# Optimization experiments

Measured on AMD Instinct MI355X. Metric: run time of the kernel, lower is better.

The kernel has to match this reference:

```python
import jax, jax.numpy as jnp
import numpy as np

B, T, H, V, S = 64, 32, 512, 32000, 400


def setup_inputs() -> dict:
    key = jax.random.key(0)
    ks = jax.random.split(key, 14)
    f = lambda k, s: jax.random.normal(k, s, dtype=jnp.float32)
    return {
        "inputs": jax.random.randint(ks[0], (B, T), 0, V),
        "embedding0": f(ks[1], (B, H)),
        "output0": f(ks[2], (B, H)),
        "tree_h0": f(ks[3], (B, H)),
        "tree_c0": f(ks[4], (B, H)),
        "tree_context": f(ks[5], (B, S, H)),
        "text_h0": f(ks[6], (B, H)),
        "text_c0": f(ks[7], (B, H)),
        "text_context": f(ks[8], (B, S, H)),
        "word_emb": f(ks[9], (V, H)) * 0.02,
        "Wx": f(ks[10], (2 * H, 4 * H)) * 0.02,   # LSTM input weights (input_size = 2H)
        "Wh": f(ks[11], (H, 4 * H)) * 0.02,       # LSTM recurrent weights
        "b": jnp.zeros((4 * H,), jnp.float32),
        "W_in": f(ks[12], (H, H)) * 0.02,         # attention score projection
        "W_out": f(ks[13], (4 * H, H)) * 0.02,    # attention combine projection
    }


def _lstm_cell(x, h, c, Wx, Wh, b):
    g = x @ Wx + h @ Wh + b                      # [B,4H]
    i, f, gg, o = jnp.split(g, 4, axis=-1)
    c_new = jax.nn.sigmoid(f) * c + jax.nn.sigmoid(i) * jnp.tanh(gg)
    h_new = jax.nn.sigmoid(o) * jnp.tanh(c_new)
    return h_new, c_new


def _attend(h, ctx, W_in):
    target = h @ W_in                             # [B,H]
    scores = jnp.einsum('bsh,bh->bs', ctx, target)
    attn = jax.nn.softmax(scores, axis=-1)
    return jnp.einsum('bs,bsh->bh', attn, ctx)    # weighted context [B,H]


def reference(inputs, embedding0, output0, tree_h0, tree_c0, tree_context,
              text_h0, text_c0, text_context, word_emb, Wx, Wh, b, W_in, W_out):
    embeddings = word_emb[inputs]                 # [B,T,H]
    embeddings = jnp.transpose(embeddings, (1, 0, 2))  # time-major [T,B,H]

    def step(carry, emb_i):
        emb, out, th, tc, xh, xc = carry
        x = jnp.concatenate([emb, out], axis=1)   # [B,2H]
        th, tc = _lstm_cell(x, th, tc, Wx, Wh, b)  # tree branch (shared weights)
        xh, xc = _lstm_cell(x, xh, xc, Wx, Wh, b)  # text branch (shared weights)
        w_tree = _attend(th, tree_context, W_in)
        w_text = _attend(xh, text_context, W_in)
        combined = jnp.concatenate([w_tree, w_text, th, xh], axis=1)  # [B,4H]
        out = jnp.tanh(combined @ W_out)           # dropout = identity (eval mode)
        return (emb_i, out, th, tc, xh, xc), out

    carry0 = (embedding0, output0, tree_h0, tree_c0, text_h0, text_c0)
    _, outs = jax.lax.scan(step, carry0, embeddings)  # outs: [T,B,H]
    return jnp.transpose(outs, (1, 0, 2))             # [B,T,H]
```

## Files before the change

kernel.cpp:

```cpp
#include <hip/hip_runtime.h>
#include <hip/hip_bf16.h>
#include <math.h>

#define BB 64
#define TT 32
#define HH 512
#define H2 1024
#define H4 2048
#define SS 400

#define OFF_WT_HI 0u
#define OFF_WT_LO 1572864u
#define OFF_WIT_HI 3145728u
#define OFF_WIT_LO 3276800u
#define OFF_EH    3407872u
#define OFF_EL    3932160u
#define OFF_OH    4456448u
#define OFF_OL    4472832u
#define OFF_HHP   4489216u
#define OFF_HLP   4521984u
#define OFF_TC    4554752u
#define OFF_XC    4620288u
#define OFF_TH    4685824u
#define OFF_XH    4751360u
#define OFF_G     4816896u
#define OFF_TGTP  6914048u
#define OFF_PACC  7438336u
#define OFF_PML   7962624u
#define OFF_CTX16 7964672u
#define WS_NEED_F 21071872u
#define OFF_WOT_HI 21071872u
#define OFF_WOT_LO 21596160u
#define OFF_COMBH  22120448u
#define OFF_COMBL  22153216u
#define WS_NEED2_F 22185984u
#define OFF_PART  OFF_G

typedef short bf16x8 __attribute__((ext_vector_type(8)));
typedef float f32x4  __attribute__((ext_vector_type(4)));

__device__ __forceinline__ float sigm(float x){ return 1.f/(1.f+__expf(-x)); }

__device__ __forceinline__ unsigned short bf_rn(float x){
  unsigned int u = __float_as_uint(x);
  return (unsigned short)((u + 0x7fffu + ((u>>16)&1u)) >> 16);
}
__device__ __forceinline__ void split2(float x, unsigned short &h, unsigned short &l){
  h = bf_rn(x);
  float hf = __uint_as_float(((unsigned int)h)<<16);
  l = bf_rn(x - hf);
}
__device__ __forceinline__ float blo(unsigned int u){ return __uint_as_float(u<<16); }
__device__ __forceinline__ float bhi(unsigned int u){ return __uint_as_float(u & 0xffff0000u); }

__global__ __launch_bounds__(256) void k_wprep(const float* __restrict__ Wx,
    const float* __restrict__ Wh, unsigned short* __restrict__ wt_hi,
    unsigned short* __restrict__ wt_lo){
  __shared__ float lds[64][68];
  int bk = blockIdx.x >> 5, bn = blockIdx.x & 31;
  int k0 = bk*64, n0 = bn*64;
  int tid = threadIdx.x;
  #pragma unroll
  for (int i=0;i<4;i++){
    int flat = tid + i*256;
    int k = flat >> 4, nq = flat & 15;
    int kg = k0 + k;
    const float* srow = (kg < 1024) ? Wx + (size_t)kg*H4 : Wh + (size_t)(kg-1024)*H4;
    float4 v = *(const float4*)(srow + n0 + nq*4);
    *(float4*)&lds[k][nq*4] = v;
  }
  __syncthreads();
  #pragma unroll
  for (int i=0;i<2;i++){
    int flat = tid + i*256;
    int n = flat >> 3, k8 = flat & 7;
    ushort4 h0, h1, l0, l1;
    unsigned short h[8], l[8];
    #pragma unroll
    for (int j=0;j<8;j++) split2(lds[k8*8+j][n], h[j], l[j]);
    h0.x=h[0];h0.y=h[1];h0.z=h[2];h0.w=h[3]; h1.x=h[4];h1.y=h[5];h1.z=h[6];h1.w=h[7];
    l0.x=l[0];l0.y=l[1];l0.z=l[2];l0.w=l[3]; l1.x=l[4];l1.y=l[5];l1.z=l[6];l1.w=l[7];
    size_t dst = (size_t)(n0+n)*1536 + k0 + k8*8;
    *(ushort4*)(wt_hi+dst) = h0; *(ushort4*)(wt_hi+dst+4) = h1;
    *(ushort4*)(wt_lo+dst) = l0; *(ushort4*)(wt_lo+dst+4) = l1;
  }
}

__global__ __launch_bounds__(256) void k_wiprep(const float* __restrict__ W_in,
    unsigned short* __restrict__ wit_hi, unsigned short* __restrict__ wit_lo){
  __shared__ float lds[64][68];
  int bk = blockIdx.x >> 3, bn = blockIdx.x & 7;
  int k0 = bk*64, n0 = bn*64;
  int tid = threadIdx.x;
  #pragma unroll
  for (int i=0;i<4;i++){
    int flat = tid + i*256;
    int k = flat >> 4, nq = flat & 15;
    float4 v = *(const float4*)(W_in + (size_t)(k0+k)*HH + n0 + nq*4);
    *(float4*)&lds[k][nq*4] = v;
  }
  __syncthreads();
  #pragma unroll
  for (int i=0;i<2;i++){
    int flat = tid + i*256;
    int n = flat >> 3, k8 = flat & 7;
    ushort4 h0, h1, l0, l1;
    unsigned short h[8], l[8];
    #pragma unroll
    for (int j=0;j<8;j++) split2(lds[k8*8+j][n], h[j], l[j]);
    h0.x=h[0];h0.y=h[1];h0.z=h[2];h0.w=h[3]; h1.x=h[4];h1.y=h[5];h1.z=h[6];h1.w=h[7];
    l0.x=l[0];l0.y=l[1];l0.z=l[2];l0.w=l[3]; l1.x=l[4];l1.y=l[5];l1.z=l[6];l1.w=l[7];
    size_t dst = (size_t)(n0+n)*HH + k0 + k8*8;
    *(ushort4*)(wit_hi+dst) = h0; *(ushort4*)(wit_hi+dst+4) = h1;
    *(ushort4*)(wit_lo+dst) = l0; *(ushort4*)(wit_lo+dst+4) = l1;
  }
}

__global__ __launch_bounds__(256) void k_woprep(const float* __restrict__ W_out,
    unsigned short* __restrict__ wot_hi, unsigned short* __restrict__ wot_lo){
  __shared__ float lds[64][68];
  int bk = blockIdx.x >> 3, bn = blockIdx.x & 7;
  int k0 = bk*64, n0 = bn*64;
  int tid = threadIdx.x;
  #pragma unroll
  for (int i=0;i<4;i++){
    int flat = tid + i*256;
    int k = flat >> 4, nq = flat & 15;
    float4 v = *(const float4*)(W_out + (size_t)(k0+k)*HH + n0 + nq*4);
    *(float4*)&lds[k][nq*4] = v;
  }
  __syncthreads();
  #pragma unroll
  for (int i=0;i<2;i++){
    int flat = tid + i*256;
    int n = flat >> 3, k8 = flat & 7;
    ushort4 h0, h1, l0, l1;
    unsigned short h[8], l[8];
    #pragma unroll
    for (int j=0;j<8;j++) split2(lds[k8*8+j][n], h[j], l[j]);
    h0.x=h[0];h0.y=h[1];h0.z=h[2];h0.w=h[3]; h1.x=h[4];h1.y=h[5];h1.z=h[6];h1.w=h[7];
    l0.x=l[0];l0.y=l[1];l0.z=l[2];l0.w=l[3]; l1.x=l[4];l1.y=l[5];l1.z=l[6];l1.w=l[7];
    size_t dst = (size_t)(n0+n)*H4 + k0 + k8*8;
    *(ushort4*)(wot_hi+dst) = h0; *(ushort4*)(wot_hi+dst+4) = h1;
    *(ushort4*)(wot_lo+dst) = l0; *(ushort4*)(wot_lo+dst+4) = l1;
  }
}

__global__ __launch_bounds__(256) void k_ctx16(const float* __restrict__ trctx,
    const float* __restrict__ txctx, unsigned short* __restrict__ ctx16){
  size_t gid = (size_t)blockIdx.x*256 + threadIdx.x;
  size_t off = gid*8;
  const size_t CH = (size_t)BB*SS*HH;
  const float* src = (off < CH) ? trctx + off : txctx + (off - CH);
  float4 a = *(const float4*)src;
  float4 c = *(const float4*)(src+4);
  ushort4 u0, u1;
  u0.x=bf_rn(a.x); u0.y=bf_rn(a.y); u0.z=bf_rn(a.z); u0.w=bf_rn(a.w);
  u1.x=bf_rn(c.x); u1.y=bf_rn(c.y); u1.z=bf_rn(c.z); u1.w=bf_rn(c.w);
  *(ushort4*)(ctx16+off) = u0;
  *(ushort4*)(ctx16+off+4) = u1;
}

__global__ __launch_bounds__(128) void k_prep(const int* __restrict__ inp,
    const float* __restrict__ emb0, const float* __restrict__ wemb,
    unsigned short* __restrict__ eh, unsigned short* __restrict__ el){
  int n = blockIdx.x; int t = n >> 6, b = n & 63;
  const float* src = (t==0) ? emb0 + (size_t)b*HH
                            : wemb + (size_t)inp[b*TT + (t-1)]*HH;
  float4 v = ((const float4*)src)[threadIdx.x];
  ushort4 h, l;
  split2(v.x,h.x,l.x); split2(v.y,h.y,l.y); split2(v.z,h.z,l.z); split2(v.w,h.w,l.w);
  size_t base = ((size_t)t*BB + b)*HH + threadIdx.x*4;
  *(ushort4*)(eh+base) = h; *(ushort4*)(el+base) = l;
}

__global__ __launch_bounds__(256) void k_init(const float* __restrict__ th0,
    const float* __restrict__ tc0, const float* __restrict__ xh0,
    const float* __restrict__ xc0, const float* __restrict__ out0,
    float* __restrict__ ws){
  unsigned short* hhp = (unsigned short*)(ws + OFF_HHP);
  unsigned short* hlp = (unsigned short*)(ws + OFF_HLP);
  unsigned short* oh  = (unsigned short*)(ws + OFF_OH);
  unsigned short* ol  = (unsigned short*)(ws + OFF_OL);
  int which = blockIdx.x >> 5;
  int idx = (blockIdx.x & 31)*256 + threadIdx.x;
  if (which==0){ ((float4*)(ws+OFF_TC))[idx] = ((const float4*)tc0)[idx]; return; }
  if (which==1){ ((float4*)(ws+OFF_XC))[idx] = ((const float4*)xc0)[idx]; return; }
  const float* s = which==2? th0 : which==3? xh0 : out0;
  float4 v = ((const float4*)s)[idx];
  ushort4 h, l;
  split2(v.x,h.x,l.x); split2(v.y,h.y,l.y); split2(v.z,h.z,l.z); split2(v.w,h.w,l.w);
  if (which==4){
    *(ushort4*)(oh + (size_t)idx*4) = h; *(ushort4*)(ol + (size_t)idx*4) = l;
  } else {
    size_t base = (size_t)(which-2)*BB*HH + (size_t)idx*4;
    *(ushort4*)(hhp+base) = h; *(ushort4*)(hlp+base) = l;
  }
}

__global__ __launch_bounds__(256) void k_gemm(const unsigned short* __restrict__ wt_hi,
    const unsigned short* __restrict__ wt_lo, const unsigned short* __restrict__ eh,
    const unsigned short* __restrict__ el, const unsigned short* __restrict__ oh,
    const unsigned short* __restrict__ ol, const unsigned short* __restrict__ hhp,
    const unsigned short* __restrict__ hlp, float* __restrict__ gpart, int t){
  int tid = threadIdx.x, lane = tid & 63, wave = tid >> 6;
  int bn = blockIdx.x & 31, ks = blockIdx.x >> 5;
  int lm = lane & 15, lk = (lane >> 4) << 3;
  f32x4 acc[2][4];
  #pragma unroll
  for (int i=0;i<2;i++)
    #pragma unroll
    for (int j=0;j<4;j++) acc[i][j] = (f32x4){0.f,0.f,0.f,0.f};
  size_t ebase[2], obase[2], hbase[2];
  #pragma unroll
  for (int i=0;i<2;i++){
    int r = (wave*2 + i)*16 + lm;
    int b = r & 63, br = r >> 6;
    ebase[i] = ((size_t)t*BB + b)*HH;
    obase[i] = (size_t)b*HH;
    hbase[i] = ((size_t)br*BB + b)*HH;
  }
  size_t wb[4];
  #pragma unroll
  for (int j=0;j<4;j++) wb[j] = (size_t)(bn*64 + j*16 + lm)*1536;
  #pragma unroll
  for (int c=0;c<6;c++){
    int kc = ks*192 + c*32;
    int sec = kc >> 9;
    int kk = (kc & 511) + lk;
    const unsigned short* ph = sec==0? eh : sec==1? oh : hhp;
    const unsigned short* pl = sec==0? el : sec==1? ol : hlp;
    bf16x8 ah[2], al[2], wh_[4], wl_[4];
    #pragma unroll
    for (int i=0;i<2;i++){
      size_t off = (sec==0? ebase[i] : sec==1? obase[i] : hbase[i]) + kk;
      ah[i] = *(const bf16x8*)(ph + off);
      al[i] = *(const bf16x8*)(pl + off);
    }
    int kw = kc + lk;
    #pragma unroll
    for (int j=0;j<4;j++){
      wh_[j] = *(const bf16x8*)(wt_hi + wb[j] + kw);
      wl_[j] = *(const bf16x8*)(wt_lo + wb[j] + kw);
    }
    #pragma unroll
    for (int i=0;i<2;i++)
      #pragma unroll
      for (int j=0;j<4;j++){
        acc[i][j] = __builtin_amdgcn_mfma_f32_16x16x32_bf16(ah[i], wh_[j], acc[i][j], 0,0,0);
        acc[i][j] = __builtin_amdgcn_mfma_f32_16x16x32_bf16(ah[i], wl_[j], acc[i][j], 0,0,0);
        acc[i][j] = __builtin_amdgcn_mfma_f32_16x16x32_bf16(al[i], wh_[j], acc[i][j], 0,0,0);
      }
  }
  int lr4 = (lane >> 4) * 4;
  #pragma unroll
  for (int i=0;i<2;i++){
    int m0 = (wave*2+i)*16;
    #pragma unroll
    for (int j=0;j<4;j++){
      int col = bn*64 + j*16 + lm;
      #pragma unroll
      for (int q=0;q<4;q++){
        int row = m0 + lr4 + q;
        gpart[((size_t)ks*128 + row)*H4 + col] = acc[i][j][q];
      }
    }
  }
}

__global__ __launch_bounds__(256) void k_lstm(float* __restrict__ ws,
    const float* __restrict__ bias, int rs){
  int gid = blockIdx.x*256 + threadIdx.x;
  int b = gid >> 9, j = gid & 511;
  int wsl = rs ^ 1;
  const float* gp = ws + OFF_G;
  unsigned short* hhp = (unsigned short*)(ws + OFF_HHP);
  unsigned short* hlp = (unsigned short*)(ws + OFF_HLP);
  #pragma unroll
  for (int br=0;br<2;br++){
    float g0=0.f,g1=0.f,g2=0.f,g3=0.f;
    #pragma unroll
    for (int ks=0;ks<8;ks++){
      size_t base = ((size_t)ks*128 + br*64 + b)*H4 + j;
      g0 += gp[base]; g1 += gp[base+512]; g2 += gp[base+1024]; g3 += gp[base+1536];
    }
    g0 += bias[j]; g1 += bias[512+j]; g2 += bias[1024+j]; g3 += bias[1536+j];
    size_t hoff = (br? OFF_XH : OFF_TH), coff = (br? OFF_XC : OFF_TC);
    float cold = ws[coff + (size_t)rs*BB*HH + (size_t)b*HH + j];
    float cn = sigm(g1)*cold + sigm(g0)*tanhf(g2);
    float hn = sigm(g3)*tanhf(cn);
    ws[coff + (size_t)wsl*BB*HH + (size_t)b*HH + j] = cn;
    ws[hoff + (size_t)wsl*BB*HH + (size_t)b*HH + j] = hn;
    unsigned short h_, l_;
    split2(hn, h_, l_);
    hhp[(size_t)(br*64+b)*HH + j] = h_;
    hlp[(size_t)(br*64+b)*HH + j] = l_;
  }
}

__global__ __launch_bounds__(256) void k_tgtB(const unsigned short* __restrict__ wit_hi,
    const unsigned short* __restrict__ wit_lo, const unsigned short* __restrict__ hhp,
    const unsigned short* __restrict__ hlp, float* __restrict__ tgtp){
  int tid = threadIdx.x, lane = tid & 63, wave = tid >> 6;
  int cn = blockIdx.x & 7, ks = blockIdx.x >> 3;
  int lm = lane & 15, lk = (lane >> 4) << 3;
  f32x4 acc[2][4];
  #pragma unroll
  for (int i=0;i<2;i++)
    #pragma unroll
    for (int j=0;j<4;j++) acc[i][j] = (f32x4){0.f,0.f,0.f,0.f};
  size_t abase[2];
  #pragma unroll
  for (int i=0;i<2;i++) abase[i] = (size_t)(wave*32 + i*16 + lm)*HH;
  size_t wb[4];
  #pragma unroll
  for (int j=0;j<4;j++) wb[j] = (size_t)(cn*64 + j*16 + lm)*HH;
  #pragma unroll
  for (int c=0;c<2;c++){
    int kc = ks*64 + c*32;
    bf16x8 ah[2], al[2], wh_[4], wl_[4];
    #pragma unroll
    for (int i=0;i<2;i++){
      ah[i] = *(const bf16x8*)(hhp + abase[i] + kc + lk);
      al[i] = *(const bf16x8*)(hlp + abase[i] + kc + lk);
    }
    #pragma unroll
    for (int j=0;j<4;j++){
      wh_[j] = *(const bf16x8*)(wit_hi + wb[j] + kc + lk);
      wl_[j] = *(const bf16x8*)(wit_lo + wb[j] + kc + lk);
    }
    #pragma unroll
    for (int i=0;i<2;i++)
      #pragma unroll
      for (int j=0;j<4;j++){
        acc[i][j] = __builtin_amdgcn_mfma_f32_16x16x32_bf16(ah[i], wh_[j], acc[i][j], 0,0,0);
        acc[i][j] = __builtin_amdgcn_mfma_f32_16x16x32_bf16(ah[i], wl_[j], acc[i][j], 0,0,0);
        acc[i][j] = __builtin_amdgcn_mfma_f32_16x16x32_bf16(al[i], wh_[j], acc[i][j], 0,0,0);
      }
  }
  int lr4 = (lane >> 4) * 4;
  #pragma unroll
  for (int i=0;i<2;i++){
    int m0 = wave*32 + i*16;
    #pragma unroll
    for (int j=0;j<4;j++){
      int col = cn*64 + j*16 + lm;
      #pragma unroll
      for (int q=0;q<4;q++){
        int row = m0 + lr4 + q;
        tgtp[((size_t)ks*128 + row)*HH + col] = acc[i][j][q];
      }
    }
  }
}

__global__ __launch_bounds__(512, 8) void k_attn(const float* __restrict__ tree_ctx,
    const float* __restrict__ text_ctx, const unsigned short* __restrict__ ctx16,
    float* __restrict__ ws, int use16){
  int blk = blockIdx.x;
  int sh = blk & 7, b = (blk>>3) & 63, branch = blk >> 9;
  int tid = threadIdx.x, lane = tid & 63, wave = tid >> 6;
  __shared__ float tgt_s[512];
  __shared__ float sc_s[64];
  __shared__ float w_s[64];
  __shared__ float accs[8][512];
  int row128 = branch*64 + b;
  if (tid < 128){
    float4 s = {0,0,0,0};
    #pragma unroll
    for (int p=0;p<8;p++){
      float4 v = *(const float4*)(ws + OFF_TGTP + ((size_t)p*128 + row128)*HH + tid*4);
      s.x += v.x; s.y += v.y; s.z += v.z; s.w += v.w;
    }
    ((float4*)tgt_s)[tid] = s;
  }
  if (tid >= 128 && tid < 192) sc_s[tid-128] = -INFINITY;
  __syncthreads();
  const size_t CH = (size_t)BB*SS*HH;
  const float* ctxf = (branch? text_ctx : tree_ctx) + ((size_t)b*SS + sh*50)*HH;
  const unsigned short* c16 = ctx16 + (branch? CH:0) + ((size_t)b*SS + sh*50)*HH;
  float4 ta = *(const float4*)&tgt_s[lane*8];
  float4 tb = *(const float4*)&tgt_s[lane*8+4];
  if (use16){
    for (int r = wave; r < 50; r += 8){
      uint4 u = *(const uint4*)(c16 + (size_t)r*HH + lane*8);
      float p = blo(u.x)*ta.x + bhi(u.x)*ta.y + blo(u.y)*ta.z + bhi(u.y)*ta.w
              + blo(u.z)*tb.x + bhi(u.z)*tb.y + blo(u.w)*tb.z + bhi(u.w)*tb.w;
      #pragma unroll
      for (int off=32; off; off>>=1) p += __shfl_xor(p, off, 64);
      if (lane==0) sc_s[r] = p;
    }
  } else {
    for (int r = wave; r < 50; r += 8){
      const float* crow = ctxf + (size_t)r*HH + lane*8;
      float4 ca = *(const float4*)crow;
      float4 cb = *(const float4*)(crow+4);
      float p = ca.x*ta.x + ca.y*ta.y + ca.z*ta.z + ca.w*ta.w
              + cb.x*tb.x + cb.y*tb.y + cb.z*tb.z + cb.w*tb.w;
      #pragma unroll
      for (int off=32; off; off>>=1) p += __shfl_xor(p, off, 64);
      if (lane==0) sc_s[r] = p;
    }
  }
  __syncthreads();
  if (wave==0){
    float s = sc_s[lane];
    float m = s;
    #pragma unroll
    for (int off=32; off; off>>=1) m = fmaxf(m, __shfl_xor(m, off, 64));
    float e = (lane<50)? __expf(s-m) : 0.f;
    w_s[lane] = e;
    float l = e;
    #pragma unroll
    for (int off=32; off; off>>=1) l += __shfl_xor(l, off, 64);
    if (lane==0){
      int pidx = (branch*64 + b)*8 + sh;
      ws[OFF_PML + (size_t)pidx*2]   = m;
      ws[OFF_PML + (size_t)pidx*2+1] = l;
    }
  }
  __syncthreads();
  float a[8] = {0,0,0,0,0,0,0,0};
  if (use16){
    for (int r = wave; r < 50; r += 8){
      float w = w_s[r];
      uint4 u = *(const uint4*)(c16 + (size_t)r*HH + lane*8);
      a[0] += w*blo(u.x); a[1] += w*bhi(u.x);
      a[2] += w*blo(u.y); a[3] += w*bhi(u.y);
      a[4] += w*blo(u.z); a[5] += w*bhi(u.z);
      a[6] += w*blo(u.w); a[7] += w*bhi(u.w);
    }
  } else {
    for (int r = wave; r < 50; r += 8){
      float w = w_s[r];
      const float* crow = ctxf + (size_t)r*HH + lane*8;
      float4 ca = *(const float4*)crow;
      float4 cb = *(const float4*)(crow+4);
      a[0] += w*ca.x; a[1] += w*ca.y; a[2] += w*ca.z; a[3] += w*ca.w;
      a[4] += w*cb.x; a[5] += w*cb.y; a[6] += w*cb.z; a[7] += w*cb.w;
    }
  }
  #pragma unroll
  for (int j=0;j<8;j++) accs[wave][lane*8+j] = a[j];
  __syncthreads();
  float s = 0.f;
  #pragma unroll
  for (int w8=0;w8<8;w8++) s += accs[w8][tid];
  int pidx = (branch*64 + b)*8 + sh;
  ws[OFF_PACC + (size_t)pidx*HH + tid] = s;
}

__global__ __launch_bounds__(256) void k_outA(float* __restrict__ ws){
  __shared__ float ce_s[2][8];
  int b = blockIdx.x, tid = threadIdx.x;
  if (tid < 2){
    int p0 = (tid*64 + b)*8;
    float mv[8], lv[8];
    float M = -INFINITY;
    #pragma unroll
    for (int i=0;i<8;i++){
      mv[i] = ws[OFF_PML + (size_t)(p0+i)*2];
      lv[i] = ws[OFF_PML + (size_t)(p0+i)*2+1];
      M = fmaxf(M, mv[i]);
    }
    float L = 0.f, ev[8];
    #pragma unroll
    for (int i=0;i<8;i++){ ev[i] = __expf(mv[i]-M); L += lv[i]*ev[i]; }
    #pragma unroll
    for (int i=0;i<8;i++) ce_s[tid][i] = ev[i]/L;
  }
  __syncthreads();
  int h = tid*4;
  int sec = h >> 9, hs = h & 511;
  int p0 = (sec*64 + b)*8;
  float4 v = {0,0,0,0};
  #pragma unroll
  for (int p=0;p<8;p++){
    float4 a = *(const float4*)(ws + OFF_PACC + (size_t)(p0+p)*HH + hs);
    float cw = ce_s[sec][p];
    v.x += a.x*cw; v.y += a.y*cw; v.z += a.z*cw; v.w += a.w*cw;
  }
  ushort4 hv, lv;
  split2(v.x,hv.x,lv.x); split2(v.y,hv.y,lv.y); split2(v.z,hv.z,lv.z); split2(v.w,hv.w,lv.w);
  unsigned short* ch = (unsigned short*)(ws + OFF_COMBH);
  unsigned short* cl = (unsigned short*)(ws + OFF_COMBL);
  *(ushort4*)(ch + (size_t)b*1024 + h) = hv;
  *(ushort4*)(cl + (size_t)b*1024 + h) = lv;
}

__global__ __launch_bounds__(256) void k_outBm(const unsigned short* __restrict__ wot_hi,
    const unsigned short* __restrict__ wot_lo, const unsigned short* __restrict__ combh,
    const unsigned short* __restrict__ combl, const unsigned short* __restrict__ hhp,
    const unsigned short* __restrict__ hlp, float* __restrict__ part){
  int tid = threadIdx.x, lane = tid & 63, wave = tid >> 6;
  int nt = blockIdx.x & 7, ks = blockIdx.x >> 3;
  int lm = lane & 15, lk = (lane >> 4) << 3;
  f32x4 acc[4];
  #pragma unroll
  for (int m=0;m<4;m++) acc[m] = (f32x4){0.f,0.f,0.f,0.f};
  size_t wb = (size_t)(nt*64 + wave*16 + lm)*H4;
  #pragma unroll
  for (int c=0;c<8;c++){
    int kg = ks*256 + c*32;
    int sec = kg >> 9;
    bf16x8 wh_ = *(const bf16x8*)(wot_hi + wb + kg + lk);
    bf16x8 wl_ = *(const bf16x8*)(wot_lo + wb + kg + lk);
    #pragma unroll
    for (int m=0;m<4;m++){
      int row = m*16 + lm;
      bf16x8 ah, al;
      if (sec < 2){
        size_t off = (size_t)row*1024 + kg + lk;
        ah = *(const bf16x8*)(combh + off);
        al = *(const bf16x8*)(combl + off);
      } else {
        size_t off = ((size_t)(sec-2)*64 + row)*HH + (kg & 511) + lk;
        ah = *(const bf16x8*)(hhp + off);
        al = *(const bf16x8*)(hlp + off);
      }
      acc[m] = __builtin_amdgcn_mfma_f32_16x16x32_bf16(ah, wh_, acc[m], 0,0,0);
      acc[m] = __builtin_amdgcn_mfma_f32_16x16x32_bf16(ah, wl_, acc[m], 0,0,0);
      acc[m] = __builtin_amdgcn_mfma_f32_16x16x32_bf16(al, wh_, acc[m], 0,0,0);
    }
  }
  int lr4 = (lane >> 4) * 4;
  int col = nt*64 + wave*16 + lm;
  #pragma unroll
  for (int m=0;m<4;m++){
    #pragma unroll
    for (int q=0;q<4;q++){
      int b = m*16 + lr4 + q;
      part[((size_t)ks*BB + b)*HH + col] = acc[m][q];
    }
  }
}

__global__ __launch_bounds__(256) void k_outB(const float* __restrict__ W_out,
    float* __restrict__ ws, int wsl){
  __shared__ float comb_s[16][256];
  __shared__ float ce_s[16][8];
  int tid = threadIdx.x, lane = tid & 63, wave = tid >> 6;
  int blk = blockIdx.x;
  int ct = blk & 7, bg = (blk>>3)&3, ks = blk>>5;
  int b0 = bg*16;
  int k0 = ks*256;
  int sec = ks >> 1;
  int kk0 = (ks & 1)*256;
  int c = ct*64 + lane;
  if (sec < 2){
    if (tid < 16){
      int b = b0 + tid;
      int p0 = (sec*64 + b)*8;
      float mv[8], lv[8];
      float M = -INFINITY;
      #pragma unroll
      for (int i=0;i<8;i++){
        mv[i] = ws[OFF_PML + (size_t)(p0+i)*2];
        lv[i] = ws[OFF_PML + (size_t)(p0+i)*2+1];
        M = fmaxf(M, mv[i]);
      }
      float L = 0.f, ev[8];
      #pragma unroll
      for (int i=0;i<8;i++){ ev[i] = __expf(mv[i]-M); L += lv[i]*ev[i]; }
      #pragma unroll
      for (int i=0;i<8;i++) ce_s[tid][i] = ev[i]/L;
    }
    __syncthreads();
  }
  #pragma unroll
  for (int i=0;i<4;i++){
    int flat = tid + i*256;
    int row = flat >> 6;
    int q   = flat & 63;
    int b = b0 + row;
    int h = kk0 + q*4;
    float4 v;
    if (sec < 2){
      int p0 = (sec*64 + b)*8;
      v.x = 0.f; v.y = 0.f; v.z = 0.f; v.w = 0.f;
      #pragma unroll
      for (int p=0;p<8;p++){
        float4 a = *(const float4*)(ws + OFF_PACC + (size_t)(p0+p)*HH + h);
        float cw = ce_s[row][p];
        v.x += a.x*cw; v.y += a.y*cw; v.z += a.z*cw; v.w += a.w*cw;
      }
    } else {
      size_t hoff = (sec==2 ? OFF_TH : OFF_XH) + (size_t)wsl*BB*HH;
      v = *(const float4*)(ws + hoff + (size_t)b*HH + h);
    }
    *(float4*)&comb_s[row][q*4] = v;
  }
  __syncthreads();
  float acc[4] = {0,0,0,0};
  #pragma unroll 4
  for (int k=0;k<256;k++){
    float wv = W_out[(size_t)(k0+k)*HH + c];
    #pragma unroll
    for (int i=0;i<4;i++) acc[i] += comb_s[wave*4+i][k]*wv;
  }
  #pragma unroll
  for (int i=0;i<4;i++){
    int b = b0 + wave*4 + i;
    ws[OFF_PART + ((size_t)ks*BB + b)*HH + c] = acc[i];
  }
}

__global__ __launch_bounds__(256) void k_outC(float* __restrict__ ws,
    float* __restrict__ dout, int t){
  int gid = blockIdx.x*256 + threadIdx.x;
  int b = gid >> 7, cq = gid & 127;
  int c0 = cq*4;
  float4 s = {0,0,0,0};
  #pragma unroll
  for (int ks=0;ks<8;ks++){
    float4 p = *(const float4*)(ws + OFF_PART + ((size_t)ks*BB + b)*HH + c0);
    s.x += p.x; s.y += p.y; s.z += p.z; s.w += p.w;
  }
  float4 o;
  o.x = tanhf(s.x); o.y = tanhf(s.y); o.z = tanhf(s.z); o.w = tanhf(s.w);
  *(float4*)(dout + ((size_t)b*TT + t)*HH + c0) = o;
  ushort4 h, l;
  split2(o.x,h.x,l.x); split2(o.y,h.y,l.y); split2(o.z,h.z,l.z); split2(o.w,h.w,l.w);
  unsigned short* oh = (unsigned short*)(ws + OFF_OH);
  unsigned short* ol = (unsigned short*)(ws + OFF_OL);
  *(ushort4*)(oh + (size_t)b*HH + c0) = h;
  *(ushort4*)(ol + (size_t)b*HH + c0) = l;
}

extern "C" void kernel_launch(void* const* d_in, const int* in_sizes, int n_in,
                              void* d_out, int out_size, void* d_ws, size_t ws_size,
                              hipStream_t stream){
  const int*   inp   = (const int*)  d_in[0];
  const float* emb0  = (const float*)d_in[1];
  const float* out0  = (const float*)d_in[2];
  const float* th0   = (const float*)d_in[3];
  const float* tc0   = (const float*)d_in[4];
  const float* trctx = (const float*)d_in[5];
  const float* xh0   = (const float*)d_in[6];
  const float* xc0   = (const float*)d_in[7];
  const float* txctx = (const float*)d_in[8];
  const float* wemb  = (const float*)d_in[9];
  const float* Wx    = (const float*)d_in[10];
  const float* Wh    = (const float*)d_in[11];
  const float* bias  = (const float*)d_in[12];
  const float* W_in  = (const float*)d_in[13];
  const float* W_out = (const float*)d_in[14];
  float* ws  = (float*)d_ws;
  float* out = (float*)d_out;
  unsigned short* wt_hi = (unsigned short*)(ws + OFF_WT_HI);
  unsigned short* wt_lo = (unsigned short*)(ws + OFF_WT_LO);
  unsigned short* wit_hi = (unsigned short*)(ws + OFF_WIT_HI);
  unsigned short* wit_lo = (unsigned short*)(ws + OFF_WIT_LO);
  unsigned short* wot_hi = (unsigned short*)(ws + OFF_WOT_HI);
  unsigned short* wot_lo = (unsigned short*)(ws + OFF_WOT_LO);
  unsigned short* combh = (unsigned short*)(ws + OFF_COMBH);
  unsigned short* combl = (unsigned short*)(ws + OFF_COMBL);
  unsigned short* eh = (unsigned short*)(ws + OFF_EH);
  unsigned short* el = (unsigned short*)(ws + OFF_EL);
  unsigned short* oh = (unsigned short*)(ws + OFF_OH);
  unsigned short* ol = (unsigned short*)(ws + OFF_OL);
  unsigned short* hhp = (unsigned short*)(ws + OFF_HHP);
  unsigned short* hlp = (unsigned short*)(ws + OFF_HLP);
  unsigned short* ctx16 = (unsigned short*)(ws + OFF_CTX16);
  float* gpart = ws + OFF_G;
  float* tgtp  = ws + OFF_TGTP;
  float* part  = ws + OFF_PART;
  int use16 = (ws_size >= (size_t)WS_NEED_F  * 4u) ? 1 : 0;
  int useMf = (ws_size >= (size_t)WS_NEED2_F * 4u) ? 1 : 0;

  hipLaunchKernelGGL(k_wprep,  dim3(768),   dim3(256), 0, stream, Wx, Wh, wt_hi, wt_lo);
  hipLaunchKernelGGL(k_wiprep, dim3(64),    dim3(256), 0, stream, W_in, wit_hi, wit_lo);
  if (useMf)
    hipLaunchKernelGGL(k_woprep, dim3(256), dim3(256), 0, stream, W_out, wot_hi, wot_lo);
  if (use16)
    hipLaunchKernelGGL(k_ctx16, dim3(12800), dim3(256), 0, stream, trctx, txctx, ctx16);
  hipLaunchKernelGGL(k_prep,   dim3(TT*BB), dim3(128), 0, stream, inp, emb0, wemb, eh, el);
  hipLaunchKernelGGL(k_init,   dim3(160),   dim3(256), 0, stream, th0, tc0, xh0, xc0, out0, ws);
  for (int t=0; t<TT; t++){
    int rs = t & 1, wsl = rs ^ 1;
    hipLaunchKernelGGL(k_gemm, dim3(256),  dim3(256), 0, stream,
                       wt_hi, wt_lo, eh, el, oh, ol, hhp, hlp, gpart, t);
    hipLaunchKernelGGL(k_lstm, dim3(128),  dim3(256), 0, stream, ws, bias, rs);
    hipLaunchKernelGGL(k_tgtB, dim3(64),   dim3(256), 0, stream, wit_hi, wit_lo, hhp, hlp, tgtp);
    hipLaunchKernelGGL(k_attn, dim3(1024), dim3(512), 0, stream, trctx, txctx, ctx16, ws, use16);
    if (useMf){
      hipLaunchKernelGGL(k_outA,  dim3(64), dim3(256), 0, stream, ws);
      hipLaunchKernelGGL(k_outBm, dim3(64), dim3(256), 0, stream,
                         wot_hi, wot_lo, combh, combl, hhp, hlp, part);
    } else {
      hipLaunchKernelGGL(k_outB, dim3(256), dim3(256), 0, stream, W_out, ws, wsl);
    }
    hipLaunchKernelGGL(k_outC, dim3(32),   dim3(256), 0, stream, ws, out, t);
  }
}
```

Baseline: 1.878 ms.

## Fuse tanh epilogue into output GEMM and drop split-K reduction kernel

The split-K output projection (64 blocks writing partial sums) plus the separate k_outC reduction and tanh kernel are replaced by one kernel. It runs 16 blocks that each loop over the full K=2048 and apply tanh in the epilogue. It writes the final output and the bf16 hi/lo split of the next-step input directly. This removes one launch per timestep and the partial-sum round trip through memory. In exchange it cuts the grid to only 16 blocks, each with a long serial K loop, which may leave most CUs idle and add latency.

New measurement: 3.342 ms. 77.9% more time.

```diff
diff --git a/kernel.cpp b/kernel.cpp
--- a/kernel.cpp
+++ b/kernel.cpp
@@ -488,49 +488,55 @@
   *(ushort4*)(cl + (size_t)b*1024 + h) = lv;
 }
 
-__global__ __launch_bounds__(256) void k_outBm(const unsigned short* __restrict__ wot_hi,
+__global__ __launch_bounds__(256) void k_outBF(const unsigned short* __restrict__ wot_hi,
     const unsigned short* __restrict__ wot_lo, const unsigned short* __restrict__ combh,
     const unsigned short* __restrict__ combl, const unsigned short* __restrict__ hhp,
-    const unsigned short* __restrict__ hlp, float* __restrict__ part){
+    const unsigned short* __restrict__ hlp, float* __restrict__ dout,
+    unsigned short* __restrict__ oh, unsigned short* __restrict__ ol, int t){
   int tid = threadIdx.x, lane = tid & 63, wave = tid >> 6;
-  int nt = blockIdx.x & 7, ks = blockIdx.x >> 3;
+  int nt = blockIdx.x & 7, mt = blockIdx.x >> 3;
   int lm = lane & 15, lk = (lane >> 4) << 3;
-  f32x4 acc[4];
-  #pragma unroll
-  for (int m=0;m<4;m++) acc[m] = (f32x4){0.f,0.f,0.f,0.f};
-  size_t wb = (size_t)(nt*64 + wave*16 + lm)*H4;
-  #pragma unroll
-  for (int c=0;c<8;c++){
-    int kg = ks*256 + c*32;
+  f32x4 acc[2];
+  acc[0] = (f32x4){0.f,0.f,0.f,0.f};
+  acc[1] = (f32x4){0.f,0.f,0.f,0.f};
+  int col = nt*64 + wave*16 + lm;
+  size_t wb = (size_t)col*H4;
+  #pragma unroll 8
+  for (int c=0;c<64;c++){
+    int kg = c*32;
     int sec = kg >> 9;
     bf16x8 wh_ = *(const bf16x8*)(wot_hi + wb + kg + lk);
     bf16x8 wl_ = *(const bf16x8*)(wot_lo + wb + kg + lk);
     #pragma unroll
-    for (int m=0;m<4;m++){
-      int row = m*16 + lm;
+    for (int mi=0;mi<2;mi++){
+      int b = mt*32 + mi*16 + lm;
       bf16x8 ah, al;
       if (sec < 2){
-        size_t off = (size_t)row*1024 + kg + lk;
+        size_t off = (size_t)b*1024 + kg + lk;
         ah = *(const bf16x8*)(combh + off);
         al = *(const bf16x8*)(combl + off);
       } else {
-        size_t off = ((size_t)(sec-2)*64 + row)*HH + (kg & 511) + lk;
+        size_t off = ((size_t)(sec-2)*64 + b)*HH + (kg & 511) + lk;
         ah = *(const bf16x8*)(hhp + off);
         al = *(const bf16x8*)(hlp + off);
       }
-      acc[m] = __builtin_amdgcn_mfma_f32_16x16x32_bf16(ah, wh_, acc[m], 0,0,0);
-      acc[m] = __builtin_amdgcn_mfma_f32_16x16x32_bf16(ah, wl_, acc[m], 0,0,0);
-      acc[m] = __builtin_amdgcn_mfma_f32_16x16x32_bf16(al, wh_, acc[m], 0,0,0);
+      acc[mi] = __builtin_amdgcn_mfma_f32_16x16x32_bf16(ah, wh_, acc[mi], 0,0,0);
+      acc[mi] = __builtin_amdgcn_mfma_f32_16x16x32_bf16(ah, wl_, acc[mi], 0,0,0);
+      acc[mi] = __builtin_amdgcn_mfma_f32_16x16x32_bf16(al, wh_, acc[mi], 0,0,0);
     }
   }
   int lr4 = (lane >> 4) * 4;
-  int col = nt*64 + wave*16 + lm;
-  #pragma unroll
-  for (int m=0;m<4;m++){
+  #pragma unroll
+  for (int mi=0;mi<2;mi++){
     #pragma unroll
     for (int q=0;q<4;q++){
-      int b = m*16 + lr4 + q;
-      part[((size_t)ks*BB + b)*HH + col] = acc[m][q];
+      int b = mt*32 + mi*16 + lr4 + q;
+      float v = tanhf(acc[mi][q]);
+      dout[((size_t)b*TT + t)*HH + col] = v;
+      unsigned short h_, l_;
+      split2(v, h_, l_);
+      oh[(size_t)b*HH + col] = h_;
+      ol[(size_t)b*HH + col] = l_;
     }
   }
 }
@@ -647,30 +653,29 @@
   const float* W_out = (const float*)d_in[14];
   float* ws  = (float*)d_ws;
   float* out = (float*)d_out;
-  unsigned short* wt_hi = (unsigned short*)(ws + OFF_WT_HI);
-  unsigned short* wt_lo = (unsigned short*)(ws + OFF_WT_LO);
+  unsigned short* wt_hi  = (unsigned short*)(ws + OFF_WT_HI);
+  unsigned short* wt_lo  = (unsigned short*)(ws + OFF_WT_LO);
   unsigned short* wit_hi = (unsigned short*)(ws + OFF_WIT_HI);
   unsigned short* wit_lo = (unsigned short*)(ws + OFF_WIT_LO);
   unsigned short* wot_hi = (unsigned short*)(ws + OFF_WOT_HI);
   unsigned short* wot_lo = (unsigned short*)(ws + OFF_WOT_LO);
-  unsigned short* combh = (unsigned short*)(ws + OFF_COMBH);
-  unsigned short* combl = (unsigned short*)(ws + OFF_COMBL);
-  unsigned short* eh = (unsigned short*)(ws + OFF_EH);
-  unsigned short* el = (unsigned short*)(ws + OFF_EL);
-  unsigned short* oh = (unsigned short*)(ws + OFF_OH);
-  unsigned short* ol = (unsigned short*)(ws + OFF_OL);
+  unsigned short* combh  = (unsigned short*)(ws + OFF_COMBH);
+  unsigned short* combl  = (unsigned short*)(ws + OFF_COMBL);
+  unsigned short* eh  = (unsigned short*)(ws + OFF_EH);
+  unsigned short* el  = (unsigned short*)(ws + OFF_EL);
+  unsigned short* oh  = (unsigned short*)(ws + OFF_OH);
+  unsigned short* ol  = (unsigned short*)(ws + OFF_OL);
   unsigned short* hhp = (unsigned short*)(ws + OFF_HHP);
   unsigned short* hlp = (unsigned short*)(ws + OFF_HLP);
   unsigned short* ctx16 = (unsigned short*)(ws + OFF_CTX16);
   float* gpart = ws + OFF_G;
   float* tgtp  = ws + OFF_TGTP;
-  float* part  = ws + OFF_PART;
   int use16 = (ws_size >= (size_t)WS_NEED_F  * 4u) ? 1 : 0;
-  int useMf = (ws_size >= (size_t)WS_NEED2_F * 4u) ? 1 : 0;
+  int fast  = (ws_size >= (size_t)WS_NEED2_F * 4u) ? 1 : 0;
 
   hipLaunchKernelGGL(k_wprep,  dim3(768),   dim3(256), 0, stream, Wx, Wh, wt_hi, wt_lo);
   hipLaunchKernelGGL(k_wiprep, dim3(64),    dim3(256), 0, stream, W_in, wit_hi, wit_lo);
-  if (useMf)
+  if (fast)
     hipLaunchKernelGGL(k_woprep, dim3(256), dim3(256), 0, stream, W_out, wot_hi, wot_lo);
   if (use16)
     hipLaunchKernelGGL(k_ctx16, dim3(12800), dim3(256), 0, stream, trctx, txctx, ctx16);
@@ -683,13 +688,13 @@
     hipLaunchKernelGGL(k_lstm, dim3(128),  dim3(256), 0, stream, ws, bias, rs);
     hipLaunchKernelGGL(k_tgtB, dim3(64),   dim3(256), 0, stream, wit_hi, wit_lo, hhp, hlp, tgtp);
     hipLaunchKernelGGL(k_attn, dim3(1024), dim3(512), 0, stream, trctx, txctx, ctx16, ws, use16);
-    if (useMf){
+    if (fast){
       hipLaunchKernelGGL(k_outA,  dim3(64), dim3(256), 0, stream, ws);
-      hipLaunchKernelGGL(k_outBm, dim3(64), dim3(256), 0, stream,
-                         wot_hi, wot_lo, combh, combl, hhp, hlp, part);
+      hipLaunchKernelGGL(k_outBF, dim3(16), dim3(256), 0, stream,
+                         wot_hi, wot_lo, combh, combl, hhp, hlp, out, oh, ol, t);
     } else {
       hipLaunchKernelGGL(k_outB, dim3(256), dim3(256), 0, stream, W_out, ws, wsl);
-    }
-    hipLaunchKernelGGL(k_outC, dim3(32),   dim3(256), 0, stream, ws, out, t);
-  }
-}
+      hipLaunchKernelGGL(k_outC, dim3(32),  dim3(256), 0, stream, ws, out, t);
+    }
+  }
+}
```
